# Optimization experiments

Measured on AMD Instinct MI355X. Metric: run time of the kernel, lower is better.

The kernel has to match this reference:

```python
import jax, jax.numpy as jnp
import numpy as np

N_SRC = 100000
N_DST = 20000
E = 1250000
D_IN = 64
D_OUT = 64
NEG_SLOPE = 0.2  # PyG GATConv default


def setup_inputs() -> dict:
    key = jax.random.key(0)
    ks = jax.random.split(key, 8)
    x = jax.random.normal(ks[0], (N_SRC, D_IN), dtype=jnp.float32)
    res_n_id = jax.random.randint(ks[1], (N_DST,), 0, N_SRC)
    edge_src = jax.random.randint(ks[2], (E,), 0, N_SRC)
    edge_dst = jax.random.randint(ks[3], (E,), 0, N_DST)
    W = jax.random.normal(ks[4], (D_IN, D_OUT), dtype=jnp.float32) / np.sqrt(D_IN)
    att_src = jax.random.normal(ks[5], (D_OUT,), dtype=jnp.float32)
    att_dst = jax.random.normal(ks[6], (D_OUT,), dtype=jnp.float32)
    bias = jax.random.normal(ks[7], (D_OUT,), dtype=jnp.float32) * 0.01
    return {"x": x, "res_n_id": res_n_id, "edge_src": edge_src,
            "edge_dst": edge_dst, "W": W, "att_src": att_src,
            "att_dst": att_dst, "bias": bias}


def reference(x, res_n_id, edge_src, edge_dst, W, att_src, att_dst, bias):
    # Shared linear transform (in_channels is an int -> one weight in PyG)
    h_src = x @ W                      # [N_src, D_OUT]
    h_dst = x[res_n_id] @ W            # [N_dst, D_OUT]
    # Per-node attention logits
    a_src = h_src @ att_src            # [N_src]
    a_dst = h_dst @ att_dst            # [N_dst]
    # Per-edge attention score (gather)
    e = jax.nn.leaky_relu(a_src[edge_src] + a_dst[edge_dst], NEG_SLOPE)  # [E]
    # Segment softmax over incoming edges of each destination node
    m = jax.ops.segment_max(e, edge_dst, num_segments=N_DST)             # [N_dst]
    ex = jnp.exp(e - m[edge_dst])
    denom = jax.ops.segment_sum(ex, edge_dst, num_segments=N_DST)        # [N_dst]
    alpha = ex / (denom[edge_dst] + 1e-16)                               # [E]
    # (dropout on alpha is eval-mode identity)
    # Weighted scatter-aggregate
    msg = h_src[edge_src] * alpha[:, None]                               # [E, D_OUT]
    out = jax.ops.segment_sum(msg, edge_dst, num_segments=N_DST)         # [N_dst, D_OUT]
    return out + bias
```

## Files before the change

kernel.cpp:

```cpp
#include <hip/hip_runtime.h>

#define N_SRC 100000
#define N_DST 20000
#define NE    1250000
#define D     64
#define NEG_SLOPE 0.2f

#define NBKT 2500
#define BCAP 768
#define TILE 4096

__device__ __forceinline__ unsigned short f2bf(float f) {
    unsigned u = __float_as_uint(f);
    u += 0x7FFFu + ((u >> 16) & 1);
    return (unsigned short)(u >> 16);
}
__device__ __forceinline__ float blo(unsigned u) { return __uint_as_float(u << 16); }
__device__ __forceinline__ float bhi(unsigned u) { return __uint_as_float(u & 0xFFFF0000u); }

__global__ void k_wad_init(const float* __restrict__ W,
                           const float* __restrict__ att_dst,
                           float* __restrict__ wad, int* __restrict__ gcur) {
    int g = blockIdx.x * 256 + threadIdx.x;
    if (g < NBKT) gcur[g] = g * BCAP;
    if (g < D) {
        float s = 0.f;
#pragma unroll
        for (int c = 0; c < D; ++c) s += W[g * D + c] * att_dst[c];
        wad[g] = s;
    }
}

__global__ __launch_bounds__(256) void k_h(const float* __restrict__ x,
                                           const float* __restrict__ W,
                                           const float* __restrict__ att_src,
                                           unsigned short* __restrict__ hb,
                                           float* __restrict__ a_src) {
    __shared__ float xs[64 * 68];
    __shared__ float Ws[64 * 64];
    int t = threadIdx.x;
    int row0 = blockIdx.x * 64;
    int nrows = N_SRC - row0; if (nrows > 64) nrows = 64;
    {
        const float4* W4 = (const float4*)W;
        float4* Ws4 = (float4*)Ws;
#pragma unroll
        for (int p = 0; p < 4; ++p) Ws4[t + 256 * p] = W4[t + 256 * p];
    }
#pragma unroll
    for (int p = 0; p < 4; ++p) {
        int idx = t + 256 * p;
        int r = idx >> 4, kq = idx & 15;
        float4 v = make_float4(0.f, 0.f, 0.f, 0.f);
        if (r < nrows) v = *(const float4*)(x + (size_t)(row0 + r) * D + 4 * kq);
        xs[(4 * kq + 0) * 68 + r] = v.x;
        xs[(4 * kq + 1) * 68 + r] = v.y;
        xs[(4 * kq + 2) * 68 + r] = v.z;
        xs[(4 * kq + 3) * 68 + r] = v.w;
    }
    __syncthreads();
    int ry = t >> 4, cx = t & 15;
    float acc[4][4] = {{0.f}};
#pragma unroll 8
    for (int k = 0; k < 64; ++k) {
        float4 xv = *(const float4*)(xs + k * 68 + 4 * ry);
        float4 wv = *(const float4*)(Ws + k * 64 + 4 * cx);
        acc[0][0] = fmaf(xv.x, wv.x, acc[0][0]); acc[0][1] = fmaf(xv.x, wv.y, acc[0][1]);
        acc[0][2] = fmaf(xv.x, wv.z, acc[0][2]); acc[0][3] = fmaf(xv.x, wv.w, acc[0][3]);
        acc[1][0] = fmaf(xv.y, wv.x, acc[1][0]); acc[1][1] = fmaf(xv.y, wv.y, acc[1][1]);
        acc[1][2] = fmaf(xv.y, wv.z, acc[1][2]); acc[1][3] = fmaf(xv.y, wv.w, acc[1][3]);
        acc[2][0] = fmaf(xv.z, wv.x, acc[2][0]); acc[2][1] = fmaf(xv.z, wv.y, acc[2][1]);
        acc[2][2] = fmaf(xv.z, wv.z, acc[2][2]); acc[2][3] = fmaf(xv.z, wv.w, acc[2][3]);
        acc[3][0] = fmaf(xv.w, wv.x, acc[3][0]); acc[3][1] = fmaf(xv.w, wv.y, acc[3][1]);
        acc[3][2] = fmaf(xv.w, wv.z, acc[3][2]); acc[3][3] = fmaf(xv.w, wv.w, acc[3][3]);
    }
    float4 a4 = *(const float4*)(att_src + 4 * cx);
#pragma unroll
    for (int j = 0; j < 4; ++j) {
        int r = 4 * ry + j;
        if (r < nrows) {
            ushort4 hv;
            hv.x = f2bf(acc[j][0]); hv.y = f2bf(acc[j][1]);
            hv.z = f2bf(acc[j][2]); hv.w = f2bf(acc[j][3]);
            *(ushort4*)(hb + (size_t)(row0 + r) * D + 4 * cx) = hv;
        }
        float p = acc[j][0] * a4.x + acc[j][1] * a4.y + acc[j][2] * a4.z + acc[j][3] * a4.w;
        p += __shfl_xor(p, 1, 64); p += __shfl_xor(p, 2, 64);
        p += __shfl_xor(p, 4, 64); p += __shfl_xor(p, 8, 64);
        if (cx == 0 && r < nrows) a_src[row0 + r] = p;
    }
}

__global__ __launch_bounds__(256) void k_adst(const float* __restrict__ x,
                                              const int* __restrict__ res_n_id,
                                              const float* __restrict__ wad,
                                              float* __restrict__ a_dst) {
    int tid = threadIdx.x;
    int wid = blockIdx.x * 4 + (tid >> 6);
    int lane = tid & 63;
    if (wid >= N_DST) return;
    int row = res_n_id[wid];
    float p = x[(size_t)row * D + lane] * wad[lane];
#pragma unroll
    for (int off = 32; off; off >>= 1) p += __shfl_xor(p, off, 64);
    if (lane == 0) a_dst[wid] = p;
}

__global__ __launch_bounds__(1024) void k_bucket(const int* __restrict__ es,
                                                 const int* __restrict__ ed,
                                                 const float* __restrict__ a_src,
                                                 const float* __restrict__ a_dst,
                                                 int* __restrict__ gcur,
                                                 int2* __restrict__ buf) {
    __shared__ int hist[NBKT];
    __shared__ int lofs[NBKT];
    __shared__ int gbase[NBKT];
    __shared__ int wtot[16];
    __shared__ int2 stage[TILE];
    int t = threadIdx.x;
    int w = t >> 6, lane = t & 63;
    int base = blockIdx.x * TILE;
    int nE = NE - base; if (nE > TILE) nE = TILE;

    for (int i = t; i < NBKT; i += 1024) hist[i] = 0;
    __syncthreads();

    int s_[4], d_[4], rk_[4];
#pragma unroll
    for (int j = 0; j < 4; ++j) {
        int i = t + 1024 * j;
        d_[j] = -1;
        if (i < nE) {
            s_[j] = es[base + i];
            d_[j] = ed[base + i];
            rk_[j] = atomicAdd(&hist[d_[j] >> 3], 1);
        }
    }
    float as_[4], ad_[4];
#pragma unroll
    for (int j = 0; j < 4; ++j) {
        if (d_[j] >= 0) { as_[j] = a_src[s_[j]]; ad_[j] = a_dst[d_[j]]; }
    }
    __syncthreads();

    int c0 = t * 3;
    int hc[3] = {0, 0, 0};
#pragma unroll
    for (int j = 0; j < 3; ++j)
        if (c0 + j < NBKT) hc[j] = hist[c0 + j];
    int sum = hc[0] + hc[1] + hc[2];
    int incl = sum;
#pragma unroll
    for (int off = 1; off < 64; off <<= 1) {
        int u = __shfl_up(incl, off, 64);
        if (lane >= off) incl += u;
    }
    if (lane == 63) wtot[w] = incl;
    __syncthreads();
    int wpre = 0;
#pragma unroll
    for (int j = 0; j < 16; ++j) wpre += (j < w) ? wtot[j] : 0;
    {
        int run = wpre + incl - sum;
#pragma unroll
        for (int j = 0; j < 3; ++j) {
            int b = c0 + j;
            if (b < NBKT) {
                lofs[b] = run;
                gbase[b] = hc[j] ? atomicAdd(&gcur[b], hc[j]) : 0;
                run += hc[j];
            }
        }
    }
    __syncthreads();

#pragma unroll
    for (int j = 0; j < 4; ++j) {
        if (d_[j] >= 0) {
            float v = as_[j] + ad_[j];
            v = v > 0.f ? v : NEG_SLOPE * v;
            float ex = __expf(v);
            int b = d_[j] >> 3;
            stage[lofs[b] + rk_[j]] =
                make_int2(s_[j] | ((d_[j] & 7) << 17) | (b << 20),
                          __float_as_int(ex));
        }
    }
    __syncthreads();

    for (int idx = t; idx < nE; idx += 1024) {
        int2 rec = stage[idx];
        int b = ((unsigned)rec.x) >> 20;
        int gpos = gbase[b] + idx - lofs[b];
        if (gpos < (b + 1) * BCAP) buf[gpos] = rec;
    }
}

__global__ __launch_bounds__(256) void k_aggB(const int2* __restrict__ buf,
                                              const int* __restrict__ gcur,
                                              const unsigned short* __restrict__ hb,
                                              const float* __restrict__ bias,
                                              float* __restrict__ out) {
    __shared__ int2 sorted[BCAP];
    __shared__ int  scw[8 * 4];
    __shared__ int  begs[9];
    int bk = blockIdx.x;
    int t = threadIdx.x;
    int w = t >> 6, lane = t & 63;
    int n = gcur[bk] - bk * BCAP;
    if (n > BCAP) n = BCAP;
    if (n < 0) n = 0;

    const int2* src = buf + (size_t)bk * BCAP;
    int2 r0 = make_int2(0, 0), r1 = make_int2(0, 0), r2 = make_int2(0, 0);
    int bin0 = -1, bin1 = -1, bin2 = -1;
    if (t < n)       { r0 = src[t];       bin0 = (r0.x >> 17) & 7; }
    if (t + 256 < n) { r1 = src[t + 256]; bin1 = (r1.x >> 17) & 7; }
    if (t + 512 < n) { r2 = src[t + 512]; bin2 = (r2.x >> 17) & 7; }

    int h[8], incl[8];
#pragma unroll
    for (int i = 0; i < 8; ++i)
        h[i] = (bin0 == i) + (bin1 == i) + (bin2 == i);

#pragma unroll
    for (int i = 0; i < 8; ++i) {
        int v = h[i];
#pragma unroll
        for (int off = 1; off < 64; off <<= 1) {
            int u = __shfl_up(v, off, 64);
            if (lane >= off) v += u;
        }
        incl[i] = v;
        int tot = __shfl(v, 63, 64);
        if (lane == 0) scw[i * 4 + w] = tot;
    }
    __syncthreads();

    if (t < 32) {
        int v = scw[t];
#pragma unroll
        for (int off = 1; off < 32; off <<= 1) {
            int u = __shfl_up(v, off, 64);
            if (t >= off) v += u;
        }
        scw[t] = v;
    }
    __syncthreads();
    if (t < 8) begs[t] = (t == 0) ? 0 : scw[t * 4 - 1];
    if (t == 8) begs[8] = n;

    int p0 = 0, p1 = 0, p2 = 0;
#pragma unroll
    for (int i = 0; i < 8; ++i) {
        int idx = i * 4 + w;
        int base_i = ((idx ? scw[idx - 1] : 0)) + (incl[i] - h[i]);
        p0 += (bin0 == i) ? base_i : 0;
        p1 += (bin1 == i) ? base_i : 0;
        p2 += (bin2 == i) ? base_i : 0;
    }
    p1 += (bin1 == bin0);
    p2 += (bin2 == bin0) + (bin2 == bin1);
    if (bin0 >= 0) sorted[p0] = r0;
    if (bin1 >= 0) sorted[p1] = r1;
    if (bin2 >= 0) sorted[p2] = r2;
    __syncthreads();

    int g = lane >> 3, il = lane & 7;
    float4 bA = *(const float4*)(bias + 8 * il);
    float4 bB = *(const float4*)(bias + 8 * il + 4);
#pragma unroll
    for (int q = 0; q < 2; ++q) {
        int dlo = w * 2 + q;
        int beg = begs[dlo], end = begs[dlo + 1];

        float a0 = 0.f, a1 = 0.f, a2 = 0.f, a3 = 0.f;
        float a4c = 0.f, a5 = 0.f, a6 = 0.f, a7 = 0.f;
        float den = 0.f;
        int i = beg;
        for (; i + 32 <= end; i += 32) {
            int2 ra = sorted[i + g];
            int2 rb = sorted[i + 8 + g];
            int2 rc = sorted[i + 16 + g];
            int2 rd = sorted[i + 24 + g];
            const uint4 ha = *(const uint4*)(hb + (size_t)(ra.x & 0x1FFFF) * D + 8 * il);
            const uint4 hc4 = *(const uint4*)(hb + (size_t)(rb.x & 0x1FFFF) * D + 8 * il);
            const uint4 he = *(const uint4*)(hb + (size_t)(rc.x & 0x1FFFF) * D + 8 * il);
            const uint4 hf = *(const uint4*)(hb + (size_t)(rd.x & 0x1FFFF) * D + 8 * il);
            float ea = __int_as_float(ra.y);
            float eb = __int_as_float(rb.y);
            float ec = __int_as_float(rc.y);
            float ed = __int_as_float(rd.y);
            a0 = fmaf(ea, blo(ha.x), a0); a1 = fmaf(ea, bhi(ha.x), a1);
            a2 = fmaf(ea, blo(ha.y), a2); a3 = fmaf(ea, bhi(ha.y), a3);
            a4c = fmaf(ea, blo(ha.z), a4c); a5 = fmaf(ea, bhi(ha.z), a5);
            a6 = fmaf(ea, blo(ha.w), a6); a7 = fmaf(ea, bhi(ha.w), a7);
            a0 = fmaf(eb, blo(hc4.x), a0); a1 = fmaf(eb, bhi(hc4.x), a1);
            a2 = fmaf(eb, blo(hc4.y), a2); a3 = fmaf(eb, bhi(hc4.y), a3);
            a4c = fmaf(eb, blo(hc4.z), a4c); a5 = fmaf(eb, bhi(hc4.z), a5);
            a6 = fmaf(eb, blo(hc4.w), a6); a7 = fmaf(eb, bhi(hc4.w), a7);
            a0 = fmaf(ec, blo(he.x), a0); a1 = fmaf(ec, bhi(he.x), a1);
            a2 = fmaf(ec, blo(he.y), a2); a3 = fmaf(ec, bhi(he.y), a3);
            a4c = fmaf(ec, blo(he.z), a4c); a5 = fmaf(ec, bhi(he.z), a5);
            a6 = fmaf(ec, blo(he.w), a6); a7 = fmaf(ec, bhi(he.w), a7);
            a0 = fmaf(ed, blo(hf.x), a0); a1 = fmaf(ed, bhi(hf.x), a1);
            a2 = fmaf(ed, blo(hf.y), a2); a3 = fmaf(ed, bhi(hf.y), a3);
            a4c = fmaf(ed, blo(hf.z), a4c); a5 = fmaf(ed, bhi(hf.z), a5);
            a6 = fmaf(ed, blo(hf.w), a6); a7 = fmaf(ed, bhi(hf.w), a7);
            den += (ea + eb) + (ec + ed);
        }
        for (; i + 16 <= end; i += 16) {
            int2 ra = sorted[i + g];
            int2 rb = sorted[i + 8 + g];
            const uint4 ha = *(const uint4*)(hb + (size_t)(ra.x & 0x1FFFF) * D + 8 * il);
            const uint4 hc4 = *(const uint4*)(hb + (size_t)(rb.x & 0x1FFFF) * D + 8 * il);
            float ea = __int_as_float(ra.y);
            float eb = __int_as_float(rb.y);
            a0 = fmaf(ea, blo(ha.x), a0); a1 = fmaf(ea, bhi(ha.x), a1);
            a2 = fmaf(ea, blo(ha.y), a2); a3 = fmaf(ea, bhi(ha.y), a3);
            a4c = fmaf(ea, blo(ha.z), a4c); a5 = fmaf(ea, bhi(ha.z), a5);
            a6 = fmaf(ea, blo(ha.w), a6); a7 = fmaf(ea, bhi(ha.w), a7);
            a0 = fmaf(eb, blo(hc4.x), a0); a1 = fmaf(eb, bhi(hc4.x), a1);
            a2 = fmaf(eb, blo(hc4.y), a2); a3 = fmaf(eb, bhi(hc4.y), a3);
            a4c = fmaf(eb, blo(hc4.z), a4c); a5 = fmaf(eb, bhi(hc4.z), a5);
            a6 = fmaf(eb, blo(hc4.w), a6); a7 = fmaf(eb, bhi(hc4.w), a7);
            den += ea + eb;
        }
        for (; i < end; i += 8) {
            int idx = i + g;
            bool ok = idx < end;
            float e = 0.f;
            if (ok) {
                int2 r = sorted[idx];
                e = __int_as_float(r.y);
                const uint4 hv = *(const uint4*)(hb + (size_t)(r.x & 0x1FFFF) * D + 8 * il);
                a0 = fmaf(e, blo(hv.x), a0); a1 = fmaf(e, bhi(hv.x), a1);
                a2 = fmaf(e, blo(hv.y), a2); a3 = fmaf(e, bhi(hv.y), a3);
                a4c = fmaf(e, blo(hv.z), a4c); a5 = fmaf(e, bhi(hv.z), a5);
                a6 = fmaf(e, blo(hv.w), a6); a7 = fmaf(e, bhi(hv.w), a7);
            }
            den += e;
        }
#pragma unroll
        for (int off = 8; off <= 32; off <<= 1) {
            a0 += __shfl_xor(a0, off, 64); a1 += __shfl_xor(a1, off, 64);
            a2 += __shfl_xor(a2, off, 64); a3 += __shfl_xor(a3, off, 64);
            a4c += __shfl_xor(a4c, off, 64); a5 += __shfl_xor(a5, off, 64);
            a6 += __shfl_xor(a6, off, 64); a7 += __shfl_xor(a7, off, 64);
            den += __shfl_xor(den, off, 64);
        }
        if (g == 0) {
            float inv = 1.f / (den + 1e-16f);
            float4 oA, oB;
            oA.x = a0 * inv + bA.x; oA.y = a1 * inv + bA.y;
            oA.z = a2 * inv + bA.z; oA.w = a3 * inv + bA.w;
            oB.x = a4c * inv + bB.x; oB.y = a5 * inv + bB.y;
            oB.z = a6 * inv + bB.z; oB.w = a7 * inv + bB.w;
            float* orow = out + ((size_t)bk * 8 + dlo) * D + 8 * il;
            *(float4*)orow = oA;
            *(float4*)(orow + 4) = oB;
        }
    }
}

extern "C" void kernel_launch(void* const* d_in, const int* in_sizes, int n_in,
                              void* d_out, int out_size, void* d_ws, size_t ws_size,
                              hipStream_t stream) {
    const float* x        = (const float*)d_in[0];
    const int*   res_n_id = (const int*)d_in[1];
    const int*   edge_src = (const int*)d_in[2];
    const int*   edge_dst = (const int*)d_in[3];
    const float* W        = (const float*)d_in[4];
    const float* att_src  = (const float*)d_in[5];
    const float* att_dst  = (const float*)d_in[6];
    const float* bias     = (const float*)d_in[7];
    float* out = (float*)d_out;

    char* w = (char*)d_ws;
    unsigned short* hb = (unsigned short*)w; w += (size_t)N_SRC * D * 2;
    int2*  buf   = (int2*)w;  w += (size_t)NBKT * BCAP * 8;
    float* a_src = (float*)w; w += (size_t)N_SRC * 4;
    float* a_dst = (float*)w; w += (size_t)N_DST * 4;
    float* wad   = (float*)w; w += 256;
    int*   gcur  = (int*)w;   w += (size_t)NBKT * 4;

    k_wad_init<<<(NBKT + 255) / 256, 256, 0, stream>>>(W, att_dst, wad, gcur);
    k_adst<<<N_DST / 4, 256, 0, stream>>>(x, res_n_id, wad, a_dst);
    k_h<<<(N_SRC + 63) / 64, 256, 0, stream>>>(x, W, att_src, hb, a_src);
    k_bucket<<<(NE + TILE - 1) / TILE, 1024, 0, stream>>>(edge_src, edge_dst, a_src, a_dst, gcur, buf);
    k_aggB<<<NBKT, 256, 0, stream>>>(buf, gcur, hb, bias, out);
}
```

Before: 172.1 us.

## Double bucket width to 16 destinations and fuse wad/a_dst prep kernels

```diff
diff --git a/kernel.cpp b/kernel.cpp
--- a/kernel.cpp
+++ b/kernel.cpp
@@ -6,8 +6,8 @@
 #define D     64
 #define NEG_SLOPE 0.2f
 
-#define NBKT 2500
-#define BCAP 768
+#define NBKT 1250
+#define BCAP 1536
 #define TILE 4096
 
 __device__ __forceinline__ unsigned short f2bf(float f) {
@@ -18,17 +18,31 @@
 __device__ __forceinline__ float blo(unsigned u) { return __uint_as_float(u << 16); }
 __device__ __forceinline__ float bhi(unsigned u) { return __uint_as_float(u & 0xFFFF0000u); }
 
-__global__ void k_wad_init(const float* __restrict__ W,
-                           const float* __restrict__ att_dst,
-                           float* __restrict__ wad, int* __restrict__ gcur) {
-    int g = blockIdx.x * 256 + threadIdx.x;
+__global__ __launch_bounds__(256) void k_prep(const float* __restrict__ W,
+                                              const float* __restrict__ att_dst,
+                                              const float* __restrict__ x,
+                                              const int* __restrict__ res_n_id,
+                                              int* __restrict__ gcur,
+                                              float* __restrict__ a_dst) {
+    __shared__ float wadL[D];
+    int t = threadIdx.x;
+    if (t < D) {
+        float s = 0.f;
+#pragma unroll
+        for (int c = 0; c < D; ++c) s += W[t * D + c] * att_dst[c];
+        wadL[t] = s;
+    }
+    int g = blockIdx.x * 256 + t;
     if (g < NBKT) gcur[g] = g * BCAP;
-    if (g < D) {
-        float s = 0.f;
-#pragma unroll
-        for (int c = 0; c < D; ++c) s += W[g * D + c] * att_dst[c];
-        wad[g] = s;
-    }
+    __syncthreads();
+    int wid = blockIdx.x * 4 + (t >> 6);
+    int lane = t & 63;
+    if (wid >= N_DST) return;
+    int row = res_n_id[wid];
+    float p = x[(size_t)row * D + lane] * wadL[lane];
+#pragma unroll
+    for (int off = 32; off; off >>= 1) p += __shfl_xor(p, off, 64);
+    if (lane == 0) a_dst[wid] = p;
 }
 
 __global__ __launch_bounds__(256) void k_h(const float* __restrict__ x,
@@ -89,21 +103,6 @@
         p += __shfl_xor(p, 4, 64); p += __shfl_xor(p, 8, 64);
         if (cx == 0 && r < nrows) a_src[row0 + r] = p;
     }
-}
-
-__global__ __launch_bounds__(256) void k_adst(const float* __restrict__ x,
-                                              const int* __restrict__ res_n_id,
-                                              const float* __restrict__ wad,
-                                              float* __restrict__ a_dst) {
-    int tid = threadIdx.x;
-    int wid = blockIdx.x * 4 + (tid >> 6);
-    int lane = tid & 63;
-    if (wid >= N_DST) return;
-    int row = res_n_id[wid];
-    float p = x[(size_t)row * D + lane] * wad[lane];
-#pragma unroll
-    for (int off = 32; off; off >>= 1) p += __shfl_xor(p, off, 64);
-    if (lane == 0) a_dst[wid] = p;
 }
 
 __global__ __launch_bounds__(1024) void k_bucket(const int* __restrict__ es,
@@ -133,7 +132,7 @@
         if (i < nE) {
             s_[j] = es[base + i];
             d_[j] = ed[base + i];
-            rk_[j] = atomicAdd(&hist[d_[j] >> 3], 1);
+            rk_[j] = atomicAdd(&hist[d_[j] >> 4], 1);
         }
     }
     float as_[4], ad_[4];
@@ -143,12 +142,10 @@
     }
     __syncthreads();
 
-    int c0 = t * 3;
-    int hc[3] = {0, 0, 0};
-#pragma unroll
-    for (int j = 0; j < 3; ++j)
-        if (c0 + j < NBKT) hc[j] = hist[c0 + j];
-    int sum = hc[0] + hc[1] + hc[2];
+    int c0 = t * 2;
+    int h0 = 0, h1 = 0;
+    if (c0 < NBKT) { h0 = hist[c0]; h1 = hist[c0 + 1]; }
+    int sum = h0 + h1;
     int incl = sum;
 #pragma unroll
     for (int off = 1; off < 64; off <<= 1) {
@@ -160,17 +157,13 @@
     int wpre = 0;
 #pragma unroll
     for (int j = 0; j < 16; ++j) wpre += (j < w) ? wtot[j] : 0;
-    {
+    if (c0 < NBKT) {
         int run = wpre + incl - sum;
-#pragma unroll
-        for (int j = 0; j < 3; ++j) {
-            int b = c0 + j;
-            if (b < NBKT) {
-                lofs[b] = run;
-                gbase[b] = hc[j] ? atomicAdd(&gcur[b], hc[j]) : 0;
-                run += hc[j];
-            }
-        }
+        lofs[c0] = run;
+        gbase[c0] = h0 ? atomicAdd(&gcur[c0], h0) : 0;
+        run += h0;
+        lofs[c0 + 1] = run;
+        gbase[c0 + 1] = h1 ? atomicAdd(&gcur[c0 + 1], h1) : 0;
     }
     __syncthreads();
 
@@ -180,9 +173,9 @@
             float v = as_[j] + ad_[j];
             v = v > 0.f ? v : NEG_SLOPE * v;
             float ex = __expf(v);
-            int b = d_[j] >> 3;
+            int b = d_[j] >> 4;
             stage[lofs[b] + rk_[j]] =
-                make_int2(s_[j] | ((d_[j] & 7) << 17) | (b << 20),
+                make_int2(s_[j] | ((d_[j] & 15) << 17) | (b << 21),
                           __float_as_int(ex));
         }
     }
@@ -190,20 +183,20 @@
 
     for (int idx = t; idx < nE; idx += 1024) {
         int2 rec = stage[idx];
-        int b = ((unsigned)rec.x) >> 20;
+        int b = ((unsigned)rec.x) >> 21;
         int gpos = gbase[b] + idx - lofs[b];
         if (gpos < (b + 1) * BCAP) buf[gpos] = rec;
     }
 }
 
-__global__ __launch_bounds__(256) void k_aggB(const int2* __restrict__ buf,
+__global__ __launch_bounds__(512) void k_aggB(const int2* __restrict__ buf,
                                               const int* __restrict__ gcur,
                                               const unsigned short* __restrict__ hb,
                                               const float* __restrict__ bias,
                                               float* __restrict__ out) {
     __shared__ int2 sorted[BCAP];
-    __shared__ int  scw[8 * 4];
-    __shared__ int  begs[9];
+    __shared__ int  scw[16 * 8];
+    __shared__ int  begs[17];
     int bk = blockIdx.x;
     int t = threadIdx.x;
     int w = t >> 6, lane = t & 63;
@@ -214,17 +207,17 @@
     const int2* src = buf + (size_t)bk * BCAP;
     int2 r0 = make_int2(0, 0), r1 = make_int2(0, 0), r2 = make_int2(0, 0);
     int bin0 = -1, bin1 = -1, bin2 = -1;
-    if (t < n)       { r0 = src[t];       bin0 = (r0.x >> 17) & 7; }
-    if (t + 256 < n) { r1 = src[t + 256]; bin1 = (r1.x >> 17) & 7; }
-    if (t + 512 < n) { r2 = src[t + 512]; bin2 = (r2.x >> 17) & 7; }
-
-    int h[8], incl[8];
-#pragma unroll
-    for (int i = 0; i < 8; ++i)
+    if (t < n)        { r0 = src[t];        bin0 = (r0.x >> 17) & 15; }
+    if (t + 512 < n)  { r1 = src[t + 512];  bin1 = (r1.x >> 17) & 15; }
+    if (t + 1024 < n) { r2 = src[t + 1024]; bin2 = (r2.x >> 17) & 15; }
+
+    int h[16], incl[16];
+#pragma unroll
+    for (int i = 0; i < 16; ++i)
         h[i] = (bin0 == i) + (bin1 == i) + (bin2 == i);
 
 #pragma unroll
-    for (int i = 0; i < 8; ++i) {
+    for (int i = 0; i < 16; ++i) {
         int v = h[i];
 #pragma unroll
         for (int off = 1; off < 64; off <<= 1) {
@@ -233,27 +226,29 @@
         }
         incl[i] = v;
         int tot = __shfl(v, 63, 64);
-        if (lane == 0) scw[i * 4 + w] = tot;
-    }
-    __syncthreads();
-
-    if (t < 32) {
+        if (lane == 0) scw[i * 8 + w] = tot;
+    }
+    __syncthreads();
+
+    if (t < 128) {
         int v = scw[t];
 #pragma unroll
-        for (int off = 1; off < 32; off <<= 1) {
+        for (int off = 1; off < 64; off <<= 1) {
             int u = __shfl_up(v, off, 64);
-            if (t >= off) v += u;
+            if ((t & 63) >= off) v += u;
         }
         scw[t] = v;
     }
     __syncthreads();
-    if (t < 8) begs[t] = (t == 0) ? 0 : scw[t * 4 - 1];
-    if (t == 8) begs[8] = n;
+    if (t >= 64 && t < 128) scw[t] += scw[63];
+    __syncthreads();
+    if (t < 16) begs[t] = (t == 0) ? 0 : scw[t * 8 - 1];
+    if (t == 16) begs[16] = n;
 
     int p0 = 0, p1 = 0, p2 = 0;
 #pragma unroll
-    for (int i = 0; i < 8; ++i) {
-        int idx = i * 4 + w;
+    for (int i = 0; i < 16; ++i) {
+        int idx = i * 8 + w;
         int base_i = ((idx ? scw[idx - 1] : 0)) + (incl[i] - h[i]);
         p0 += (bin0 == i) ? base_i : 0;
         p1 += (bin1 == i) ? base_i : 0;
@@ -356,7 +351,7 @@
             oA.z = a2 * inv + bA.z; oA.w = a3 * inv + bA.w;
             oB.x = a4c * inv + bB.x; oB.y = a5 * inv + bB.y;
             oB.z = a6 * inv + bB.z; oB.w = a7 * inv + bB.w;
-            float* orow = out + ((size_t)bk * 8 + dlo) * D + 8 * il;
+            float* orow = out + ((size_t)bk * 16 + dlo) * D + 8 * il;
             *(float4*)orow = oA;
             *(float4*)(orow + 4) = oB;
         }
@@ -381,12 +376,10 @@
     int2*  buf   = (int2*)w;  w += (size_t)NBKT * BCAP * 8;
     float* a_src = (float*)w; w += (size_t)N_SRC * 4;
     float* a_dst = (float*)w; w += (size_t)N_DST * 4;
-    float* wad   = (float*)w; w += 256;
     int*   gcur  = (int*)w;   w += (size_t)NBKT * 4;
 
-    k_wad_init<<<(NBKT + 255) / 256, 256, 0, stream>>>(W, att_dst, wad, gcur);
-    k_adst<<<N_DST / 4, 256, 0, stream>>>(x, res_n_id, wad, a_dst);
+    k_prep<<<N_DST / 4, 256, 0, stream>>>(W, att_dst, x, res_n_id, gcur, a_dst);
     k_h<<<(N_SRC + 63) / 64, 256, 0, stream>>>(x, W, att_src, hb, a_src);
     k_bucket<<<(NE + TILE - 1) / TILE, 1024, 0, stream>>>(edge_src, edge_dst, a_src, a_dst, gcur, buf);
-    k_aggB<<<NBKT, 256, 0, stream>>>(buf, gcur, hb, bias, out);
-}
+    k_aggB<<<NBKT, 512, 0, stream>>>(buf, gcur, hb, bias, out);
+}
```

Measured after the change: 174.6 us. No clear change (+1.4%).
